# Performance work log

Measured on AMD Instinct MI355X. Metric: run time of the kernel, lower is better.

## Reference

```python
import jax, jax.numpy as jnp
import numpy as np

B, D, H = 262144, 3, 64


def _mlp(params, x):
    # x: [D] -> scalar u
    (W1, b1), (W2, b2), (W3, b3), (W4, b4) = params
    h = jnp.tanh(x @ W1 + b1)
    h = jnp.tanh(h @ W2 + b2)
    h = jnp.tanh(h @ W3 + b3)
    return (h @ W4 + b4)[0]


def setup_inputs() -> dict:
    key = jax.random.key(0)
    ks = jax.random.split(key, 6)
    def glorot(k, shape):
        fan_in = shape[0]
        return jax.random.normal(k, shape, dtype=jnp.float32) / jnp.sqrt(jnp.float32(fan_in))
    return {
        "x_r": jax.random.normal(ks[0], (B, D), dtype=jnp.float32),
        "sigma_r": jax.random.uniform(ks[1], (B,), dtype=jnp.float32),
        "W1": glorot(ks[2], (D, H)), "b1": jnp.zeros((H,), jnp.float32),
        "W2": glorot(ks[3], (H, H)), "b2": jnp.zeros((H,), jnp.float32),
        "W3": glorot(ks[4], (H, H)), "b3": jnp.zeros((H,), jnp.float32),
        "W4": glorot(ks[5], (H, 1)), "b4": jnp.zeros((1,), jnp.float32),
    }


def reference(x_r, sigma_r, W1, b1, W2, b2, W3, b3, W4, b4):
    # r(x) = div( sigma * grad u(x) ) = trace( d(flux)/dx ), per sample.
    params = ((W1, b1), (W2, b2), (W3, b3), (W4, b4))

    def flux_single(x, s):
        # sigma * grad_u, shape [D]
        return s * jax.grad(lambda xx: _mlp(params, xx))(x)

    def div_single(x, s):
        # forward-over-reverse: jacfwd of reverse-mode grad -> [D, D]; take trace
        J = jax.jacfwd(lambda xx: flux_single(xx, s))(x)
        return jnp.trace(J)

    div = jax.vmap(div_single)(x_r, sigma_r)  # [B]
    return div[:, None]
```

## Files before the change

### kernel.cpp

```cpp
#include <hip/hip_runtime.h>

typedef __fp16 f16;
typedef f16  h8 __attribute__((ext_vector_type(8)));
typedef float f4 __attribute__((ext_vector_type(4)));

#define WPB 4
#define SPW 16
#define BTOT 262144
#define NBLOCKS (BTOT / (WPB * SPW))

union H8u { h8 v; unsigned u[4]; };

__device__ __forceinline__ unsigned pk2(float a, float b) {
    return __builtin_bit_cast(unsigned, __builtin_amdgcn_cvt_pkrtz(a, b));
}

__device__ __forceinline__ void tanh_sech2(float a, float& h, float& g) {
    float ac = fminf(fmaxf(a, -15.f), 15.f);
    float E = __expf(2.f * ac);
    float inv = __builtin_amdgcn_rcpf(E + 1.f);
    h = 1.f - 2.f * inv;
    g = 4.f * E * inv * inv;
}

__global__ __launch_bounds__(256, 2) void pinn_mfma_kernel(
    const float* __restrict__ x_r, const float* __restrict__ sigma_r,
    const float* __restrict__ W1, const float* __restrict__ b1,
    const float* __restrict__ W2, const float* __restrict__ b2,
    const float* __restrict__ W3, const float* __restrict__ b3,
    const float* __restrict__ W4, float* __restrict__ out)
{
    __shared__ f4 Wp[64];
    __shared__ float Q1l[64];
    __shared__ f4 B2l[16], B3l[16], W4l[16];
    __shared__ __align__(16) float xch[WPB][2][16 * 68];

    const int tid  = threadIdx.x;
    const int lane = tid & 63;
    const int wv   = tid >> 6;
    const int sb   = lane & 15;
    const int q    = lane >> 4;

    if (tid < 64) {
        float wx = W1[tid], wy = W1[64 + tid], wz = W1[128 + tid];
        f4 w; w[0] = wx; w[1] = wy; w[2] = wz; w[3] = b1[tid];
        Wp[tid] = w;
        Q1l[tid] = wx * wx + wy * wy + wz * wz;
        ((float*)B2l)[tid] = b2[tid];
        ((float*)B3l)[tid] = b3[tid];
        ((float*)W4l)[tid] = W4[tid];
    }
    __syncthreads();

    h8 A2f[4][2], A3f[4][2];
#pragma unroll
    for (int mt = 0; mt < 4; ++mt)
#pragma unroll
    for (int kk = 0; kk < 2; ++kk) {
        H8u t2, t3;
#pragma unroll
        for (int p = 0; p < 4; ++p) {
            const int r0 = (32 * kk + 8 * q + 2 * p) * 64 + 16 * mt + sb;
            t2.u[p] = pk2(W2[r0], W2[r0 + 64]);
            t3.u[p] = pk2(W3[r0], W3[r0 + 64]);
        }
        A2f[mt][kk] = t2.v; A3f[mt][kk] = t3.v;
    }

    const long s = ((long)blockIdx.x * WPB + wv) * SPW + sb;
    const float x0 = x_r[s * 3], x1 = x_r[s * 3 + 1], x2 = x_r[s * 3 + 2];
    const float sg = sigma_r[s];

    h8 Bh[2], Bx[2], By[2], Bz[2], Bs[2];
#pragma unroll
    for (int kk = 0; kk < 2; ++kk) {
        H8u th, tx, ty, tz, ts;
#pragma unroll
        for (int p = 0; p < 4; ++p) {
            float hv[2], xv[2], yv[2], zv[2], sv[2];
#pragma unroll
            for (int o = 0; o < 2; ++o) {
                const int u = 32 * kk + 8 * q + 2 * p + o;
                f4 w = Wp[u];
                float a = fmaf(w[0], x0, fmaf(w[1], x1, fmaf(w[2], x2, w[3])));
                float h, g; tanh_sech2(a, h, g);
                hv[o] = h; xv[o] = g * w[0]; yv[o] = g * w[1]; zv[o] = g * w[2];
                sv[o] = -2.f * h * g * Q1l[u];
            }
            th.u[p] = pk2(hv[0], hv[1]); tx.u[p] = pk2(xv[0], xv[1]);
            ty.u[p] = pk2(yv[0], yv[1]); tz.u[p] = pk2(zv[0], zv[1]);
            ts.u[p] = pk2(sv[0], sv[1]);
        }
        Bh[kk] = th.v; Bx[kk] = tx.v; By[kk] = ty.v; Bz[kk] = tz.v; Bs[kk] = ts.v;
    }

    f4 Ch[4], Cx[4], Cy[4], Cz[4], Cs[4];
#pragma unroll
    for (int mt = 0; mt < 4; ++mt) {
        Ch[mt] = (f4){0.f,0.f,0.f,0.f}; Cx[mt] = (f4){0.f,0.f,0.f,0.f};
        Cy[mt] = (f4){0.f,0.f,0.f,0.f}; Cz[mt] = (f4){0.f,0.f,0.f,0.f};
        Cs[mt] = (f4){0.f,0.f,0.f,0.f};
    }
#pragma unroll
    for (int mt = 0; mt < 4; ++mt)
#pragma unroll
    for (int kk = 0; kk < 2; ++kk) {
        Ch[mt] = __builtin_amdgcn_mfma_f32_16x16x32_f16(A2f[mt][kk], Bh[kk], Ch[mt], 0, 0, 0);
        Cx[mt] = __builtin_amdgcn_mfma_f32_16x16x32_f16(A2f[mt][kk], Bx[kk], Cx[mt], 0, 0, 0);
        Cy[mt] = __builtin_amdgcn_mfma_f32_16x16x32_f16(A2f[mt][kk], By[kk], Cy[mt], 0, 0, 0);
        Cz[mt] = __builtin_amdgcn_mfma_f32_16x16x32_f16(A2f[mt][kk], Bz[kk], Cz[mt], 0, 0, 0);
        Cs[mt] = __builtin_amdgcn_mfma_f32_16x16x32_f16(A2f[mt][kk], Bs[kk], Cs[mt], 0, 0, 0);
    }

    f4 Oh[4], Ox[4], Oy[4], Oz[4], Os[4];
#pragma unroll
    for (int mt = 0; mt < 4; ++mt) {
        f4 bb = B2l[4 * mt + q];
#pragma unroll
        for (int r = 0; r < 4; ++r) {
            float a = Ch[mt][r] + bb[r];
            float h, g; tanh_sech2(a, h, g);
            float ax = Cx[mt][r], ay = Cy[mt][r], az = Cz[mt][r];
            Oh[mt][r] = h; Ox[mt][r] = g * ax; Oy[mt][r] = g * ay; Oz[mt][r] = g * az;
            Os[mt][r] = fmaf(g, Cs[mt][r], -2.f * h * g * (ax * ax + ay * ay + az * az));
        }
    }

    f4* xb0 = (f4*)&xch[wv][0][0];
    f4* xb1 = (f4*)&xch[wv][1][0];
    const int wo = sb * 17 + q;
    const int ro = sb * 17 + 2 * q;

#define XWR(bufp, O) { bufp[wo] = O[0]; bufp[wo + 4] = O[1]; bufp[wo + 8] = O[2]; bufp[wo + 12] = O[3]; }
#define XRD(bufp, Bf) { f4 r0 = bufp[ro], r1 = bufp[ro + 1], r2 = bufp[ro + 8], r3 = bufp[ro + 9]; \
        H8u t0, t1; \
        t0.u[0] = pk2(r0[0], r0[1]); t0.u[1] = pk2(r0[2], r0[3]); \
        t0.u[2] = pk2(r1[0], r1[1]); t0.u[3] = pk2(r1[2], r1[3]); \
        t1.u[0] = pk2(r2[0], r2[1]); t1.u[1] = pk2(r2[2], r2[3]); \
        t1.u[2] = pk2(r3[0], r3[1]); t1.u[3] = pk2(r3[2], r3[3]); \
        Bf[0] = t0.v; Bf[1] = t1.v; }

    XWR(xb0, Oh)
    XWR(xb1, Ox)
    XRD(xb0, Bh)
    XWR(xb0, Oy)
    XRD(xb1, Bx)
    XWR(xb1, Oz)
    XRD(xb0, By)
    XWR(xb0, Os)
    XRD(xb1, Bz)
    XRD(xb0, Bs)

#pragma unroll
    for (int mt = 0; mt < 4; ++mt) {
        Ch[mt] = (f4){0.f,0.f,0.f,0.f}; Cx[mt] = (f4){0.f,0.f,0.f,0.f};
        Cy[mt] = (f4){0.f,0.f,0.f,0.f}; Cz[mt] = (f4){0.f,0.f,0.f,0.f};
        Cs[mt] = (f4){0.f,0.f,0.f,0.f};
    }
#pragma unroll
    for (int mt = 0; mt < 4; ++mt)
#pragma unroll
    for (int kk = 0; kk < 2; ++kk) {
        Ch[mt] = __builtin_amdgcn_mfma_f32_16x16x32_f16(A3f[mt][kk], Bh[kk], Ch[mt], 0, 0, 0);
        Cx[mt] = __builtin_amdgcn_mfma_f32_16x16x32_f16(A3f[mt][kk], Bx[kk], Cx[mt], 0, 0, 0);
        Cy[mt] = __builtin_amdgcn_mfma_f32_16x16x32_f16(A3f[mt][kk], By[kk], Cy[mt], 0, 0, 0);
        Cz[mt] = __builtin_amdgcn_mfma_f32_16x16x32_f16(A3f[mt][kk], Bz[kk], Cz[mt], 0, 0, 0);
        Cs[mt] = __builtin_amdgcn_mfma_f32_16x16x32_f16(A3f[mt][kk], Bs[kk], Cs[mt], 0, 0, 0);
    }

    float tot = 0.f;
#pragma unroll
    for (int mt = 0; mt < 4; ++mt) {
        f4 bb = B3l[4 * mt + q], w4v = W4l[4 * mt + q];
#pragma unroll
        for (int r = 0; r < 4; ++r) {
            float a = Ch[mt][r] + bb[r];
            float h, g; tanh_sech2(a, h, g);
            float ax = Cx[mt][r], ay = Cy[mt][r], az = Cz[mt][r];
            float sv = fmaf(g, Cs[mt][r], -2.f * h * g * (ax * ax + ay * ay + az * az));
            tot = fmaf(sv, w4v[r], tot);
        }
    }
    tot += __shfl_xor(tot, 16);
    tot += __shfl_xor(tot, 32);
    if (lane < 16) out[s] = sg * tot;
}

extern "C" void kernel_launch(void* const* d_in, const int* in_sizes, int n_in,
                              void* d_out, int out_size, void* d_ws, size_t ws_size,
                              hipStream_t stream) {
    const float* x_r     = (const float*)d_in[0];
    const float* sigma_r = (const float*)d_in[1];
    const float* W1      = (const float*)d_in[2];
    const float* b1      = (const float*)d_in[3];
    const float* W2      = (const float*)d_in[4];
    const float* b2      = (const float*)d_in[5];
    const float* W3      = (const float*)d_in[6];
    const float* b3      = (const float*)d_in[7];
    const float* W4      = (const float*)d_in[8];
    float* out = (float*)d_out;

    pinn_mfma_kernel<<<NBLOCKS, 256, 0, stream>>>(
        x_r, sigma_r, W1, b1, W2, b2, W3, b3, W4, out);
}
```

Baseline: 49.90 us.

## Loop each wave over four sample batches with prefetch and fp16 LDS exchange

Each wave now processes 64 samples in four batches of 16 inside a loop. The MFMA weight fragments for W2 and W3 are therefore loaded once and reused across batches, and the next batch's inputs are prefetched during the current one. The layer-1 activations now also go through an LDS exchange stored as packed fp16, and MFMAs and epilogue work are interleaved per output tile so fewer accumulators are live. The tanh clamp is removed, sech² is computed with fewer operations, and occupancy is raised to 3 blocks. The risks are more LDS traffic for layer 1, a serial dependency chain inside the loop, and possible overflow of exp for large inputs.

```diff
diff --git a/kernel.cpp b/kernel.cpp
--- a/kernel.cpp
+++ b/kernel.cpp
@@ -3,52 +3,54 @@
 typedef __fp16 f16;
 typedef f16  h8 __attribute__((ext_vector_type(8)));
 typedef float f4 __attribute__((ext_vector_type(4)));
+typedef unsigned u32t;
 
+#define NBLOCKS 1024
 #define WPB 4
-#define SPW 16
-#define BTOT 262144
-#define NBLOCKS (BTOT / (WPB * SPW))
+#define SPW 64
+#define NBATCH 4
+#define XSTR 36
+#define XST  (16 * XSTR)
 
-union H8u { h8 v; unsigned u[4]; };
+union H8u { h8 v; u32t u[4]; };
+union U4h { uint4 u; h8 v; };
 
-__device__ __forceinline__ unsigned pk2(float a, float b) {
-    return __builtin_bit_cast(unsigned, __builtin_amdgcn_cvt_pkrtz(a, b));
+__device__ __forceinline__ u32t pk2(float a, float b) {
+    return __builtin_bit_cast(u32t, __builtin_amdgcn_cvt_pkrtz(a, b));
 }
 
 __device__ __forceinline__ void tanh_sech2(float a, float& h, float& g) {
-    float ac = fminf(fmaxf(a, -15.f), 15.f);
-    float E = __expf(2.f * ac);
+    float E = __expf(2.f * a);
     float inv = __builtin_amdgcn_rcpf(E + 1.f);
-    h = 1.f - 2.f * inv;
-    g = 4.f * E * inv * inv;
+    float u = inv + inv;
+    h = 1.f - u;
+    g = u * (2.f - u);
 }
 
-__global__ __launch_bounds__(256, 2) void pinn_mfma_kernel(
+__global__ __launch_bounds__(256, 3) void pinn_mfma_kernel(
     const float* __restrict__ x_r, const float* __restrict__ sigma_r,
     const float* __restrict__ W1, const float* __restrict__ b1,
     const float* __restrict__ W2, const float* __restrict__ b2,
     const float* __restrict__ W3, const float* __restrict__ b3,
     const float* __restrict__ W4, float* __restrict__ out)
 {
-    __shared__ f4 Wp[64];
-    __shared__ float Q1l[64];
-    __shared__ f4 B2l[16], B3l[16], W4l[16];
-    __shared__ __align__(16) float xch[WPB][2][16 * 68];
+    __shared__ f4 Wg[64];
+    __shared__ f4 Wb4[16], B2v[16], B3v[16], W4v[16];
+    __shared__ u32t xch[WPB][5 * XST];
 
-    const int tid  = threadIdx.x;
-    const int lane = tid & 63;
-    const int wv   = tid >> 6;
-    const int sb   = lane & 15;
-    const int q    = lane >> 4;
+    const int tid = threadIdx.x, lane = tid & 63, wv = tid >> 6;
+    const int sb = lane & 15;
+    const int q  = lane >> 4;
 
     if (tid < 64) {
         float wx = W1[tid], wy = W1[64 + tid], wz = W1[128 + tid];
-        f4 w; w[0] = wx; w[1] = wy; w[2] = wz; w[3] = b1[tid];
-        Wp[tid] = w;
-        Q1l[tid] = wx * wx + wy * wy + wz * wz;
-        ((float*)B2l)[tid] = b2[tid];
-        ((float*)B3l)[tid] = b3[tid];
-        ((float*)W4l)[tid] = W4[tid];
+        f4 w; w[0] = wx; w[1] = wy; w[2] = wz;
+        w[3] = -2.f * (wx * wx + wy * wy + wz * wz);
+        Wg[tid] = w;
+        ((float*)Wb4)[tid] = b1[tid];
+        ((float*)B2v)[tid] = b2[tid];
+        ((float*)B3v)[tid] = b3[tid];
+        ((float*)W4v)[tid] = W4[tid];
     }
     __syncthreads();
 
@@ -67,123 +69,103 @@
         A2f[mt][kk] = t2.v; A3f[mt][kk] = t3.v;
     }
 
-    const long s = ((long)blockIdx.x * WPB + wv) * SPW + sb;
-    const float x0 = x_r[s * 3], x1 = x_r[s * 3 + 1], x2 = x_r[s * 3 + 2];
-    const float sg = sigma_r[s];
+    u32t* xb = xch[wv];
+    const int wbase = sb * XSTR + 2 * q;
+    const int rbase = sb * XSTR + 4 * q;
 
-    h8 Bh[2], Bx[2], By[2], Bz[2], Bs[2];
-#pragma unroll
-    for (int kk = 0; kk < 2; ++kk) {
-        H8u th, tx, ty, tz, ts;
-#pragma unroll
-        for (int p = 0; p < 4; ++p) {
-            float hv[2], xv[2], yv[2], zv[2], sv[2];
-#pragma unroll
-            for (int o = 0; o < 2; ++o) {
-                const int u = 32 * kk + 8 * q + 2 * p + o;
-                f4 w = Wp[u];
-                float a = fmaf(w[0], x0, fmaf(w[1], x1, fmaf(w[2], x2, w[3])));
-                float h, g; tanh_sech2(a, h, g);
-                hv[o] = h; xv[o] = g * w[0]; yv[o] = g * w[1]; zv[o] = g * w[2];
-                sv[o] = -2.f * h * g * Q1l[u];
-            }
-            th.u[p] = pk2(hv[0], hv[1]); tx.u[p] = pk2(xv[0], xv[1]);
-            ty.u[p] = pk2(yv[0], yv[1]); tz.u[p] = pk2(zv[0], zv[1]);
-            ts.u[p] = pk2(sv[0], sv[1]);
-        }
-        Bh[kk] = th.v; Bx[kk] = tx.v; By[kk] = ty.v; Bz[kk] = tz.v; Bs[kk] = ts.v;
+    const long sbase = ((long)blockIdx.x * WPB + wv) * SPW;
+
+    float nx0 = x_r[(sbase + sb) * 3], nx1 = x_r[(sbase + sb) * 3 + 1],
+          nx2 = x_r[(sbase + sb) * 3 + 2], nsg = sigma_r[sbase + sb];
+
+#define WR5(mt) { const int wo = wbase + 8 * (mt);                                         \
+    *(uint2*)&xb[0 * XST + wo] = make_uint2(pk2(oh[0], oh[1]), pk2(oh[2], oh[3]));         \
+    *(uint2*)&xb[1 * XST + wo] = make_uint2(pk2(ox[0], ox[1]), pk2(ox[2], ox[3]));         \
+    *(uint2*)&xb[2 * XST + wo] = make_uint2(pk2(oy[0], oy[1]), pk2(oy[2], oy[3]));         \
+    *(uint2*)&xb[3 * XST + wo] = make_uint2(pk2(oz[0], oz[1]), pk2(oz[2], oz[3]));         \
+    *(uint2*)&xb[4 * XST + wo] = make_uint2(pk2(os[0], os[1]), pk2(os[2], os[3])); }
+
+#define RDB(Bf, st) { U4h u0, u1;                                                          \
+    u0.u = *(const uint4*)&xb[(st) * XST + rbase];                                         \
+    u1.u = *(const uint4*)&xb[(st) * XST + rbase + 16];                                    \
+    Bf[0] = u0.v; Bf[1] = u1.v; }
+
+#define MFMA10(Af) _Pragma("unroll")                                                       \
+    for (int kk = 0; kk < 2; ++kk) {                                                       \
+        Ch = __builtin_amdgcn_mfma_f32_16x16x32_f16(Af[mt][kk], Bh[kk], Ch, 0, 0, 0);      \
+        Cx = __builtin_amdgcn_mfma_f32_16x16x32_f16(Af[mt][kk], Bx[kk], Cx, 0, 0, 0);      \
+        Cy = __builtin_amdgcn_mfma_f32_16x16x32_f16(Af[mt][kk], By[kk], Cy, 0, 0, 0);      \
+        Cz = __builtin_amdgcn_mfma_f32_16x16x32_f16(Af[mt][kk], Bz[kk], Cz, 0, 0, 0);      \
+        Cs = __builtin_amdgcn_mfma_f32_16x16x32_f16(Af[mt][kk], Bs[kk], Cs, 0, 0, 0);      \
     }
 
-    f4 Ch[4], Cx[4], Cy[4], Cz[4], Cs[4];
-#pragma unroll
-    for (int mt = 0; mt < 4; ++mt) {
-        Ch[mt] = (f4){0.f,0.f,0.f,0.f}; Cx[mt] = (f4){0.f,0.f,0.f,0.f};
-        Cy[mt] = (f4){0.f,0.f,0.f,0.f}; Cz[mt] = (f4){0.f,0.f,0.f,0.f};
-        Cs[mt] = (f4){0.f,0.f,0.f,0.f};
-    }
-#pragma unroll
-    for (int mt = 0; mt < 4; ++mt)
-#pragma unroll
-    for (int kk = 0; kk < 2; ++kk) {
-        Ch[mt] = __builtin_amdgcn_mfma_f32_16x16x32_f16(A2f[mt][kk], Bh[kk], Ch[mt], 0, 0, 0);
-        Cx[mt] = __builtin_amdgcn_mfma_f32_16x16x32_f16(A2f[mt][kk], Bx[kk], Cx[mt], 0, 0, 0);
-        Cy[mt] = __builtin_amdgcn_mfma_f32_16x16x32_f16(A2f[mt][kk], By[kk], Cy[mt], 0, 0, 0);
-        Cz[mt] = __builtin_amdgcn_mfma_f32_16x16x32_f16(A2f[mt][kk], Bz[kk], Cz[mt], 0, 0, 0);
-        Cs[mt] = __builtin_amdgcn_mfma_f32_16x16x32_f16(A2f[mt][kk], Bs[kk], Cs[mt], 0, 0, 0);
-    }
-
-    f4 Oh[4], Ox[4], Oy[4], Oz[4], Os[4];
-#pragma unroll
-    for (int mt = 0; mt < 4; ++mt) {
-        f4 bb = B2l[4 * mt + q];
-#pragma unroll
-        for (int r = 0; r < 4; ++r) {
-            float a = Ch[mt][r] + bb[r];
-            float h, g; tanh_sech2(a, h, g);
-            float ax = Cx[mt][r], ay = Cy[mt][r], az = Cz[mt][r];
-            Oh[mt][r] = h; Ox[mt][r] = g * ax; Oy[mt][r] = g * ay; Oz[mt][r] = g * az;
-            Os[mt][r] = fmaf(g, Cs[mt][r], -2.f * h * g * (ax * ax + ay * ay + az * az));
-        }
-    }
-
-    f4* xb0 = (f4*)&xch[wv][0][0];
-    f4* xb1 = (f4*)&xch[wv][1][0];
-    const int wo = sb * 17 + q;
-    const int ro = sb * 17 + 2 * q;
-
-#define XWR(bufp, O) { bufp[wo] = O[0]; bufp[wo + 4] = O[1]; bufp[wo + 8] = O[2]; bufp[wo + 12] = O[3]; }
-#define XRD(bufp, Bf) { f4 r0 = bufp[ro], r1 = bufp[ro + 1], r2 = bufp[ro + 8], r3 = bufp[ro + 9]; \
-        H8u t0, t1; \
-        t0.u[0] = pk2(r0[0], r0[1]); t0.u[1] = pk2(r0[2], r0[3]); \
-        t0.u[2] = pk2(r1[0], r1[1]); t0.u[3] = pk2(r1[2], r1[3]); \
-        t1.u[0] = pk2(r2[0], r2[1]); t1.u[1] = pk2(r2[2], r2[3]); \
-        t1.u[2] = pk2(r3[0], r3[1]); t1.u[3] = pk2(r3[2], r3[3]); \
-        Bf[0] = t0.v; Bf[1] = t1.v; }
-
-    XWR(xb0, Oh)
-    XWR(xb1, Ox)
-    XRD(xb0, Bh)
-    XWR(xb0, Oy)
-    XRD(xb1, Bx)
-    XWR(xb1, Oz)
-    XRD(xb0, By)
-    XWR(xb0, Os)
-    XRD(xb1, Bz)
-    XRD(xb0, Bs)
+#pragma unroll 1
+    for (int t = 0; t < NBATCH; ++t) {
+        const float x0 = nx0, x1 = nx1, x2 = nx2, sg = nsg;
+        const long sn = sbase + ((t + 1) & 3) * 16 + sb;
+        nx0 = x_r[sn * 3]; nx1 = x_r[sn * 3 + 1]; nx2 = x_r[sn * 3 + 2];
+        nsg = sigma_r[sn];
 
 #pragma unroll
-    for (int mt = 0; mt < 4; ++mt) {
-        Ch[mt] = (f4){0.f,0.f,0.f,0.f}; Cx[mt] = (f4){0.f,0.f,0.f,0.f};
-        Cy[mt] = (f4){0.f,0.f,0.f,0.f}; Cz[mt] = (f4){0.f,0.f,0.f,0.f};
-        Cs[mt] = (f4){0.f,0.f,0.f,0.f};
+        for (int mt = 0; mt < 4; ++mt) {
+            const f4 bb = Wb4[4 * mt + q];
+            float oh[4], ox[4], oy[4], oz[4], os[4];
+#pragma unroll
+            for (int r = 0; r < 4; ++r) {
+                const f4 w = Wg[16 * mt + 4 * q + r];
+                float a = fmaf(w[0], x0, fmaf(w[1], x1, fmaf(w[2], x2, bb[r])));
+                float h, g; tanh_sech2(a, h, g);
+                oh[r] = h; ox[r] = g * w[0]; oy[r] = g * w[1]; oz[r] = g * w[2];
+                os[r] = (h * g) * w[3];
+            }
+            WR5(mt)
+        }
+
+        h8 Bh[2], Bx[2], By[2], Bz[2], Bs[2];
+        RDB(Bh, 0) RDB(Bx, 1) RDB(By, 2) RDB(Bz, 3) RDB(Bs, 4)
+
+#pragma unroll
+        for (int mt = 0; mt < 4; ++mt) {
+            f4 Ch = {0.f,0.f,0.f,0.f}, Cx = {0.f,0.f,0.f,0.f}, Cy = {0.f,0.f,0.f,0.f},
+               Cz = {0.f,0.f,0.f,0.f}, Cs = {0.f,0.f,0.f,0.f};
+            MFMA10(A2f)
+            const f4 bb = B2v[4 * mt + q];
+            float oh[4], ox[4], oy[4], oz[4], os[4];
+#pragma unroll
+            for (int r = 0; r < 4; ++r) {
+                float h, g; tanh_sech2(Ch[r] + bb[r], h, g);
+                float ax = Cx[r], ay = Cy[r], az = Cz[r];
+                float qq  = fmaf(ax, ax, fmaf(ay, ay, az * az));
+                float hg2 = (h * g) * 2.f;
+                oh[r] = h; ox[r] = g * ax; oy[r] = g * ay; oz[r] = g * az;
+                os[r] = fmaf(g, Cs[r], -(hg2 * qq));
+            }
+            WR5(mt)
+        }
+
+        RDB(Bh, 0) RDB(Bx, 1) RDB(By, 2) RDB(Bz, 3) RDB(Bs, 4)
+
+        float tot = 0.f;
+#pragma unroll
+        for (int mt = 0; mt < 4; ++mt) {
+            f4 Ch = {0.f,0.f,0.f,0.f}, Cx = {0.f,0.f,0.f,0.f}, Cy = {0.f,0.f,0.f,0.f},
+               Cz = {0.f,0.f,0.f,0.f}, Cs = {0.f,0.f,0.f,0.f};
+            MFMA10(A3f)
+            const f4 bb = B3v[4 * mt + q], w4 = W4v[4 * mt + q];
+#pragma unroll
+            for (int r = 0; r < 4; ++r) {
+                float h, g; tanh_sech2(Ch[r] + bb[r], h, g);
+                float ax = Cx[r], ay = Cy[r], az = Cz[r];
+                float qq  = fmaf(ax, ax, fmaf(ay, ay, az * az));
+                float hg2 = (h * g) * 2.f;
+                float sv  = fmaf(g, Cs[r], -(hg2 * qq));
+                tot = fmaf(sv, w4[r], tot);
+            }
+        }
+        tot += __shfl_xor(tot, 16);
+        tot += __shfl_xor(tot, 32);
+        if (lane < 16) out[sbase + t * 16 + sb] = sg * tot;
     }
-#pragma unroll
-    for (int mt = 0; mt < 4; ++mt)
-#pragma unroll
-    for (int kk = 0; kk < 2; ++kk) {
-        Ch[mt] = __builtin_amdgcn_mfma_f32_16x16x32_f16(A3f[mt][kk], Bh[kk], Ch[mt], 0, 0, 0);
-        Cx[mt] = __builtin_amdgcn_mfma_f32_16x16x32_f16(A3f[mt][kk], Bx[kk], Cx[mt], 0, 0, 0);
-        Cy[mt] = __builtin_amdgcn_mfma_f32_16x16x32_f16(A3f[mt][kk], By[kk], Cy[mt], 0, 0, 0);
-        Cz[mt] = __builtin_amdgcn_mfma_f32_16x16x32_f16(A3f[mt][kk], Bz[kk], Cz[mt], 0, 0, 0);
-        Cs[mt] = __builtin_amdgcn_mfma_f32_16x16x32_f16(A3f[mt][kk], Bs[kk], Cs[mt], 0, 0, 0);
-    }
-
-    float tot = 0.f;
-#pragma unroll
-    for (int mt = 0; mt < 4; ++mt) {
-        f4 bb = B3l[4 * mt + q], w4v = W4l[4 * mt + q];
-#pragma unroll
-        for (int r = 0; r < 4; ++r) {
-            float a = Ch[mt][r] + bb[r];
-            float h, g; tanh_sech2(a, h, g);
-            float ax = Cx[mt][r], ay = Cy[mt][r], az = Cz[mt][r];
-            float sv = fmaf(g, Cs[mt][r], -2.f * h * g * (ax * ax + ay * ay + az * az));
-            tot = fmaf(sv, w4v[r], tot);
-        }
-    }
-    tot += __shfl_xor(tot, 16);
-    tot += __shfl_xor(tot, 32);
-    if (lane < 16) out[s] = sg * tot;
 }
 
 extern "C" void kernel_launch(void* const* d_in, const int* in_sizes, int n_in,
```

Measured after the change: 44.14 us. 1.13x faster.
